# Performance work log

Measured on AMD Instinct MI355X. Metric: run time of the kernel, lower is better.

Reference implementation:

```python
import jax, jax.numpy as jnp
import numpy as np

B, IDF, CDF, IH, IW, SL = 32, 768, 768, 32, 32, 128

def setup_inputs() -> dict:
    key = jax.random.key(0)
    k1, k2, k3, k4 = jax.random.split(key, 4)
    inp = jax.random.normal(k1, (B, IDF, IH, IW), dtype=jnp.float32)
    ctx = jax.random.normal(k2, (B, CDF, SL), dtype=jnp.float32)
    mask = jax.random.randint(k3, (B, SL), 0, 2, dtype=jnp.int32)
    # 1x1 conv with no bias == matmul weight [idf, cdf]
    w_conv = jax.random.normal(k4, (IDF, CDF), dtype=jnp.float32) * 0.02
    return {"input": inp, "context": ctx, "mask": mask, "w_conv": w_conv}

def reference(input, context, mask, w_conv):
    b, idf, ih, iw = input.shape
    queryL = ih * iw
    sourceL = context.shape[2]
    # target: b x idf x queryL
    target = input.reshape(b, idf, queryL)
    # 1x1 conv projection of context: b x idf x sourceL
    sourceT = jnp.einsum('oc,bcs->bos', w_conv, context)
    # attention logits: b x queryL x sourceL (targetT @ sourceT)
    attn = jnp.einsum('biq,bis->bqs', target, sourceT)
    attn = attn + mask[:, None, :].astype(attn.dtype) * (-10000.0)
    attn = jax.nn.softmax(attn, axis=-1)  # softmax over sourceL
    # weighted context: sourceT @ attn^T -> b x idf x queryL
    weightedContext = jnp.einsum('bis,bqs->biq', sourceT, attn).reshape(b, idf, ih, iw)
    attn_out = jnp.transpose(attn, (0, 2, 1)).reshape(b, sourceL, ih, iw)
    return weightedContext, attn_out
```

## Files before the change

kernel.cpp:

```cpp
#include <hip/hip_runtime.h>

#define NB  32
#define IDF 768
#define SLN 128
#define QLN 1024
#define NT  24
#define NT2 12

typedef _Float16 v8hf __attribute__((ext_vector_type(8)));
typedef _Float16 v4hf __attribute__((ext_vector_type(4)));
typedef float    v4f  __attribute__((ext_vector_type(4)));

#define MFMAH __builtin_amdgcn_mfma_f32_16x16x32_f16

__device__ __forceinline__ void gload16(const void* g, void* l) {
  __builtin_amdgcn_global_load_lds(
      (const __attribute__((address_space(1))) void*)g,
      (__attribute__((address_space(3))) void*)l, 16, 0, 0);
}

__device__ __forceinline__ void lbar() {
  asm volatile("s_waitcnt lgkmcnt(0)" ::: "memory");
  __builtin_amdgcn_sched_barrier(0);
  __builtin_amdgcn_s_barrier();
  __builtin_amdgcn_sched_barrier(0);
}

__global__ __launch_bounds__(256) void prep_k(const float* __restrict__ W,
                                              const float* __restrict__ ctx,
                                              _Float16* __restrict__ Wf,
                                              _Float16* __restrict__ cTf) {
  const int bid = blockIdx.x, t = threadIdx.x;
  __shared__ float tl[64][133];
  if (bid < 576) {
    int idx = bid * 1024 + t * 4;
    float4 v = *(const float4*)(W + idx);
    v4hf h;
    h[0] = (_Float16)v.x;
    h[1] = (_Float16)v.y;
    h[2] = (_Float16)v.z;
    h[3] = (_Float16)v.w;
    *(v4hf*)(Wf + idx) = h;
    return;
  }
  const int cid = bid - 576;
  const int b = cid / 12, c0 = (cid % 12) * 64;
#pragma unroll
  for (int j = 0; j < 8; ++j) {
    int u = j * 256 + t;
    int c = u >> 5, s4 = (u & 31) * 4;
    *(float4*)&tl[c][s4] =
        *(const float4*)(ctx + ((size_t)b * IDF + c0 + c) * SLN + s4);
  }
  __syncthreads();
#pragma unroll
  for (int j = 0; j < 8; ++j) {
    int u = j * 256 + t;
    int s = u >> 4, c4 = (u & 15) * 4;
    v4hf h;
#pragma unroll
    for (int e = 0; e < 4; ++e) h[e] = (_Float16)tl[c4 + e][s];
    *(v4hf*)(cTf + ((size_t)b * SLN + s) * IDF + c0 + c4) = h;
  }
}

__global__ __launch_bounds__(256) void proj_k(const _Float16* __restrict__ cTf,
                                              const _Float16* __restrict__ Wf,
                                              _Float16* __restrict__ STf,
                                              _Float16* __restrict__ Shvf) {
  const int b = blockIdx.y, o0 = blockIdx.x * 32;
  const int t = threadIdx.x, w = t >> 6, lane = t & 63;
  const int lr = lane & 15, lg = lane >> 4;
  const int ws = w >> 1, wq = w & 1;
  __shared__ _Float16 AL[128][32];

  v4f acc[4];
#pragma unroll
  for (int fr = 0; fr < 4; ++fr) acc[fr] = (v4f){0.f, 0.f, 0.f, 0.f};

  const int ra = t >> 1, ca0 = (t & 1) * 2;
  const int swA = (ra >> 1) & 3;
  const int pa0 = (ca0 ^ swA) * 8, pa1 = ((ca0 + 1) ^ swA) * 8;
  const _Float16* pA = cTf + ((size_t)b * SLN + ra) * IDF + ca0 * 8;
  const size_t wOff = (size_t)(o0 + wq * 16 + lr) * IDF + lg * 8;

  uint4 aA0, aA1, bA0, bA1;
  v8hf bhc, bhn;
  aA0 = *(const uint4*)(pA);
  aA1 = *(const uint4*)(pA + 8);
  bA0 = *(const uint4*)(pA + 32);
  bA1 = *(const uint4*)(pA + 40);
  bhc = *(const v8hf*)(Wf + wOff);

#define PROJ_BODY(S0, S1, IT)                                                  \
  {                                                                            \
    lbar();                                                                    \
    *(uint4*)&AL[ra][pa0] = S0;                                                \
    *(uint4*)&AL[ra][pa1] = S1;                                                \
    if ((IT) + 2 < NT) {                                                       \
      S0 = *(const uint4*)(pA + ((IT) + 2) * 32);                              \
      S1 = *(const uint4*)(pA + ((IT) + 2) * 32 + 8);                          \
    }                                                                          \
    if ((IT) + 1 < NT) {                                                       \
      bhn = *(const v8hf*)(Wf + wOff + ((IT) + 1) * 32);                       \
    }                                                                          \
    lbar();                                                                    \
    _Pragma("unroll") for (int fr = 0; fr < 4; ++fr) {                         \
      const int r = ws * 64 + fr * 16 + lr;                                    \
      const int pp = (lg ^ ((r >> 1) & 3)) * 8;                                \
      v8hf ah = *(const v8hf*)&AL[r][pp];                                      \
      acc[fr] = MFMAH(ah, bhc, acc[fr], 0, 0, 0);                              \
    }                                                                          \
    bhc = bhn;                                                                 \
  }

  for (int it2 = 0; it2 < NT / 2; ++it2) {
    const int itE = it2 * 2;
    PROJ_BODY(aA0, aA1, itE);
    PROJ_BODY(bA0, bA1, itE + 1);
  }
#undef PROJ_BODY

  const int o = o0 + wq * 16 + lr;
#pragma unroll
  for (int fr = 0; fr < 4; ++fr) {
    v4hf hp;
#pragma unroll
    for (int r = 0; r < 4; ++r) {
      int s = ws * 64 + fr * 16 + lg * 4 + r;
      _Float16 h = (_Float16)acc[fr][r];
      STf[((size_t)b * SLN + s) * IDF + o] = h;
      hp[r] = h;
    }
    *(v4hf*)(Shvf + ((size_t)b * IDF + o) * SLN + ws * 64 + fr * 16 + lg * 4) =
        hp;
  }
}

__global__ __launch_bounds__(256, 4) void qkpv_k(const float* __restrict__ input,
                                                 const _Float16* __restrict__ STf,
                                                 const _Float16* __restrict__ Shvf,
                                                 const int* __restrict__ mask,
                                                 float* __restrict__ wc,
                                                 float* __restrict__ attn_out) {
  const int bid = blockIdx.x;
  const int nid = (bid & 7) * 64 + (bid >> 3);
  const int b = nid >> 4, q0 = (nid & 15) * 64;
  const int t = threadIdx.x, w = t >> 6, lane = t & 63;
  const int lr = lane & 15, lg = lane >> 4;
  const int wqp = w & 1, sh2 = w >> 1;

  __shared__ __align__(16) char lds[34304];
  float* const msk  = (float*)(lds + 32768);
  float* const redm = (float*)(lds + 33280);
  float* const reds = (float*)(lds + 33792);
  char* const PLb = lds;

  if (t < SLN) msk[t] = -10000.0f * (float)mask[b * SLN + t];

  v4f acc[4][2];
#pragma unroll
  for (int fr = 0; fr < 4; ++fr)
#pragma unroll
    for (int j = 0; j < 2; ++j) acc[fr][j] = (v4f){0.f, 0.f, 0.f, 0.f};

  const int rA = (lane >> 3);
  const int cpA = lane & 7;
  const _Float16* gA[4];
#pragma unroll
  for (int g = 0; g < 4; ++g) {
    const int row = w * 32 + g * 8 + rA;
    const int c = cpA ^ (row & 7);
    gA[g] = STf + ((size_t)b * SLN + row) * IDF + c * 8;
  }
  const int dA = w * 4096;

  const float* gB = input + (size_t)b * IDF * QLN + q0 + wqp * 32 + lr;

#pragma unroll
  for (int g = 0; g < 4; ++g) gload16(gA[g], lds + dA + g * 1024);
  v8hf aH[2][2], bH[2][2];
  float tmpB[2][2][8];
#pragma unroll
  for (int kk = 0; kk < 2; ++kk)
#pragma unroll
    for (int j = 0; j < 2; ++j)
#pragma unroll
      for (int e = 0; e < 8; ++e)
        tmpB[kk][j][e] = gB[(size_t)(kk * 32 + lg * 8 + e) * QLN + j * 16];
#pragma unroll
  for (int kk = 0; kk < 2; ++kk)
#pragma unroll
    for (int j = 0; j < 2; ++j)
#pragma unroll
      for (int e = 0; e < 8; ++e) aH[kk][j][e] = (_Float16)tmpB[kk][j][e];
#pragma unroll
  for (int g = 0; g < 4; ++g) gload16(gA[g] + 64, lds + 16384 + dA + g * 1024);

#define QK_WIN(CUROFF, BC, BN, IT, VMC)                                        \
  {                                                                            \
    asm volatile("s_waitcnt vmcnt(" #VMC ")" ::: "memory");                    \
    __builtin_amdgcn_sched_barrier(0);                                         \
    __builtin_amdgcn_s_barrier();                                              \
    __builtin_amdgcn_sched_barrier(0);                                         \
    if ((IT) + 1 < NT2) {                                                      \
      _Pragma("unroll") for (int kk = 0; kk < 2; ++kk)                         \
          _Pragma("unroll") for (int j = 0; j < 2; ++j)                        \
          _Pragma("unroll") for (int e = 0; e < 8; ++e)                        \
          tmpB[kk][j][e] =                                                     \
              gB[(size_t)(((IT) + 1) * 64 + kk * 32 + lg * 8 + e) * QLN +      \
                 j * 16];                                                      \
    }                                                                          \
    __builtin_amdgcn_sched_barrier(0);                                         \
    const char* Ab = lds + (CUROFF);                                           \
    __builtin_amdgcn_s_setprio(1);                                             \
    _Pragma("unroll") for (int fr = 0; fr < 4; ++fr) {                         \
      const int r = sh2 * 64 + fr * 16 + lr;                                   \
      _Pragma("unroll") for (int kk = 0; kk < 2; ++kk) {                       \
        const int cc = (kk * 4 + lg) ^ (r & 7);                                \
        v8hf ah = *(const v8hf*)(Ab + r * 128 + cc * 16);                      \
        _Pragma("unroll") for (int j = 0; j < 2; ++j) {                        \
          acc[fr][j] = MFMAH(ah, BC[kk][j], acc[fr][j], 0, 0, 0);              \
        }                                                                      \
      }                                                                        \
    }                                                                          \
    __builtin_amdgcn_s_setprio(0);                                             \
    __builtin_amdgcn_sched_barrier(0);                                         \
    if ((IT) + 1 < NT2) {                                                      \
      _Pragma("unroll") for (int kk = 0; kk < 2; ++kk)                         \
          _Pragma("unroll") for (int j = 0; j < 2; ++j)                        \
          _Pragma("unroll") for (int e = 0; e < 8; ++e)                        \
          BN[kk][j][e] = (_Float16)tmpB[kk][j][e];                             \
    }                                                                          \
    asm volatile("s_waitcnt lgkmcnt(0)" ::: "memory");                         \
    __builtin_amdgcn_s_barrier();                                              \
    if ((IT) + 2 < NT2) {                                                      \
      _Pragma("unroll") for (int g = 0; g < 4; ++g)                            \
          gload16(gA[g] + (size_t)((IT) + 2) * 64,                             \
                  lds + (CUROFF) + dA + g * 1024);                             \
    }                                                                          \
  }

  for (int it2 = 0; it2 < 5; ++it2) {
    const int itE = it2 * 2;
    QK_WIN(0, aH, bH, itE, 4);
    QK_WIN(16384, bH, aH, itE + 1, 4);
  }
  QK_WIN(0, aH, bH, 10, 4);
  QK_WIN(16384, bH, aH, 11, 0);
#undef QK_WIN

  float mx[2], sum[2];
#pragma unroll
  for (int j = 0; j < 2; ++j) {
    mx[j] = -3.0e38f;
#pragma unroll
    for (int fr = 0; fr < 4; ++fr)
#pragma unroll
      for (int r = 0; r < 4; ++r) {
        acc[fr][j][r] += msk[sh2 * 64 + fr * 16 + lg * 4 + r];
        mx[j] = fmaxf(mx[j], acc[fr][j][r]);
      }
    mx[j] = fmaxf(mx[j], __shfl_xor(mx[j], 16));
    mx[j] = fmaxf(mx[j], __shfl_xor(mx[j], 32));
    if (lg == 0) redm[sh2 * 64 + wqp * 32 + j * 16 + lr] = mx[j];
  }
  __syncthreads();
#pragma unroll
  for (int j = 0; j < 2; ++j) {
    const int qh = wqp * 32 + j * 16 + lr;
    mx[j] = fmaxf(redm[qh], redm[64 + qh]);
    sum[j] = 0.f;
#pragma unroll
    for (int fr = 0; fr < 4; ++fr)
#pragma unroll
      for (int r = 0; r < 4; ++r) {
        float e = __expf(acc[fr][j][r] - mx[j]);
        acc[fr][j][r] = e;
        sum[j] += e;
      }
    sum[j] += __shfl_xor(sum[j], 16);
    sum[j] += __shfl_xor(sum[j], 32);
    if (lg == 0) reds[sh2 * 64 + wqp * 32 + j * 16 + lr] = sum[j];
  }
  __syncthreads();
#pragma unroll
  for (int j = 0; j < 2; ++j) {
    const int qh = wqp * 32 + j * 16 + lr;
    const float inv = 1.0f / (reds[qh] + reds[64 + qh]);
    const int q = q0 + qh;
#pragma unroll
    for (int fr = 0; fr < 4; ++fr) {
      v4hf hp;
#pragma unroll
      for (int r = 0; r < 4; ++r) {
        float p = acc[fr][j][r] * inv;
        attn_out[((size_t)b * SLN + sh2 * 64 + fr * 16 + lg * 4 + r) * QLN + q] =
            p;
        hp[r] = (_Float16)p;
      }
      const int g = (sh2 * 8 + fr * 2 + (lg >> 1)) ^ lr;
      *(v4hf*)(PLb + qh * 256 + g * 16 + (lg & 1) * 8) = hp;
    }
  }
  __syncthreads();

  const int qfp = (w & 1) * 2;
  const int islab = (w >> 1) * 384;
  v8hf pa0v[4], pa1v[4];
#pragma unroll
  for (int kt = 0; kt < 4; ++kt) {
    const int g0 = (kt * 4 + lg) ^ lr;
    pa0v[kt] = *(const v8hf*)(PLb + (qfp * 16 + lr) * 256 + g0 * 16);
    pa1v[kt] = *(const v8hf*)(PLb + ((qfp + 1) * 16 + lr) * 256 + g0 * 16);
  }
  const _Float16* pShv = Shvf + ((size_t)b * IDF + islab + lr) * SLN + lg * 8;
  float* pWc = wc + ((size_t)b * IDF + islab + lr) * QLN + q0;
#pragma unroll 2
  for (int ifr = 0; ifr < 24; ++ifr) {
    v4f a0 = (v4f){0.f, 0.f, 0.f, 0.f};
    v4f a1 = (v4f){0.f, 0.f, 0.f, 0.f};
#pragma unroll
    for (int kt = 0; kt < 4; ++kt) {
      v8hf bb = *(const v8hf*)(pShv + (size_t)(ifr * 16) * SLN + kt * 32);
      a0 = MFMAH(pa0v[kt], bb, a0, 0, 0, 0);
      a1 = MFMAH(pa1v[kt], bb, a1, 0, 0, 0);
    }
    *(float4*)(pWc + (size_t)(ifr * 16) * QLN + qfp * 16 + lg * 4) =
        make_float4(a0[0], a0[1], a0[2], a0[3]);
    *(float4*)(pWc + (size_t)(ifr * 16) * QLN + (qfp + 1) * 16 + lg * 4) =
        make_float4(a1[0], a1[1], a1[2], a1[3]);
  }
}

extern "C" void kernel_launch(void* const* d_in, const int* in_sizes, int n_in,
                              void* d_out, int out_size, void* d_ws, size_t ws_size,
                              hipStream_t stream) {
  const float* input   = (const float*)d_in[0];
  const float* context = (const float*)d_in[1];
  const int*   mask    = (const int*)d_in[2];
  const float* w_conv  = (const float*)d_in[3];

  float* out      = (float*)d_out;
  float* wc       = out;
  float* attn_out = out + (size_t)NB * IDF * QLN;

  const size_t SE = (size_t)NB * SLN * IDF;
  _Float16* wsb = (_Float16*)d_ws;
  _Float16* STf  = wsb;
  _Float16* Shvf = STf + SE;
  _Float16* scr  = (_Float16*)wc;
  _Float16* cTf  = scr;
  _Float16* Wf   = cTf + SE;

  prep_k<<<960, 256, 0, stream>>>(w_conv, context, Wf, cTf);
  proj_k<<<dim3(24, NB), 256, 0, stream>>>(cTf, Wf, STf, Shvf);
  qkpv_k<<<512, 256, 0, stream>>>(input, STf, Shvf, mask, wc, attn_out);
}
```

Baseline: 81.16 us.

## Halve query tile per block to 32 and double grid to 1024 blocks

The fused QK-softmax-PV kernel now handles 32 query positions per block instead of 64, so the launch doubles to 1024 blocks and per-thread accumulators and B-fragment registers halve. This aims to raise occupancy and balance work across the many compute units. In exchange, each block reloads the full STf and Shvf slices for its batch, doubling their global/L2 traffic, and each block does fewer MFMAs per LDS/global load.

```diff
diff --git a/kernel.cpp b/kernel.cpp
--- a/kernel.cpp
+++ b/kernel.cpp
@@ -144,25 +144,23 @@
                                                  float* __restrict__ wc,
                                                  float* __restrict__ attn_out) {
   const int bid = blockIdx.x;
-  const int nid = (bid & 7) * 64 + (bid >> 3);
-  const int b = nid >> 4, q0 = (nid & 15) * 64;
+  const int nid = (bid & 7) * 128 + (bid >> 3);
+  const int b = nid >> 5, q0 = (nid & 31) * 32;
   const int t = threadIdx.x, w = t >> 6, lane = t & 63;
   const int lr = lane & 15, lg = lane >> 4;
-  const int wqp = w & 1, sh2 = w >> 1;
-
-  __shared__ __align__(16) char lds[34304];
+  const int wq = w & 1, sh2 = w >> 1;
+
+  __shared__ __align__(16) char lds[33792];
   float* const msk  = (float*)(lds + 32768);
   float* const redm = (float*)(lds + 33280);
-  float* const reds = (float*)(lds + 33792);
+  float* const reds = (float*)(lds + 33536);
   char* const PLb = lds;
 
   if (t < SLN) msk[t] = -10000.0f * (float)mask[b * SLN + t];
 
-  v4f acc[4][2];
-#pragma unroll
-  for (int fr = 0; fr < 4; ++fr)
-#pragma unroll
-    for (int j = 0; j < 2; ++j) acc[fr][j] = (v4f){0.f, 0.f, 0.f, 0.f};
+  v4f acc[4];
+#pragma unroll
+  for (int fr = 0; fr < 4; ++fr) acc[fr] = (v4f){0.f, 0.f, 0.f, 0.f};
 
   const int rA = (lane >> 3);
   const int cpA = lane & 7;
@@ -175,25 +173,21 @@
   }
   const int dA = w * 4096;
 
-  const float* gB = input + (size_t)b * IDF * QLN + q0 + wqp * 32 + lr;
+  const float* gB = input + (size_t)b * IDF * QLN + q0 + wq * 16 + lr;
 
 #pragma unroll
   for (int g = 0; g < 4; ++g) gload16(gA[g], lds + dA + g * 1024);
-  v8hf aH[2][2], bH[2][2];
-  float tmpB[2][2][8];
+  v8hf aH[2], bH[2];
+  float tmpB[2][8];
 #pragma unroll
   for (int kk = 0; kk < 2; ++kk)
 #pragma unroll
-    for (int j = 0; j < 2; ++j)
-#pragma unroll
-      for (int e = 0; e < 8; ++e)
-        tmpB[kk][j][e] = gB[(size_t)(kk * 32 + lg * 8 + e) * QLN + j * 16];
+    for (int e = 0; e < 8; ++e)
+      tmpB[kk][e] = gB[(size_t)(kk * 32 + lg * 8 + e) * QLN];
 #pragma unroll
   for (int kk = 0; kk < 2; ++kk)
 #pragma unroll
-    for (int j = 0; j < 2; ++j)
-#pragma unroll
-      for (int e = 0; e < 8; ++e) aH[kk][j][e] = (_Float16)tmpB[kk][j][e];
+    for (int e = 0; e < 8; ++e) aH[kk][e] = (_Float16)tmpB[kk][e];
 #pragma unroll
   for (int g = 0; g < 4; ++g) gload16(gA[g] + 64, lds + 16384 + dA + g * 1024);
 
@@ -205,11 +199,9 @@
     __builtin_amdgcn_sched_barrier(0);                                         \
     if ((IT) + 1 < NT2) {                                                      \
       _Pragma("unroll") for (int kk = 0; kk < 2; ++kk)                         \
-          _Pragma("unroll") for (int j = 0; j < 2; ++j)                        \
           _Pragma("unroll") for (int e = 0; e < 8; ++e)                        \
-          tmpB[kk][j][e] =                                                     \
-              gB[(size_t)(((IT) + 1) * 64 + kk * 32 + lg * 8 + e) * QLN +      \
-                 j * 16];                                                      \
+          tmpB[kk][e] =                                                        \
+              gB[(size_t)(((IT) + 1) * 64 + kk * 32 + lg * 8 + e) * QLN];      \
     }                                                                          \
     __builtin_amdgcn_sched_barrier(0);                                         \
     const char* Ab = lds + (CUROFF);                                           \
@@ -219,18 +211,15 @@
       _Pragma("unroll") for (int kk = 0; kk < 2; ++kk) {                       \
         const int cc = (kk * 4 + lg) ^ (r & 7);                                \
         v8hf ah = *(const v8hf*)(Ab + r * 128 + cc * 16);                      \
-        _Pragma("unroll") for (int j = 0; j < 2; ++j) {                        \
-          acc[fr][j] = MFMAH(ah, BC[kk][j], acc[fr][j], 0, 0, 0);              \
-        }                                                                      \
+        acc[fr] = MFMAH(ah, BC[kk], acc[fr], 0, 0, 0);                         \
       }                                                                        \
     }                                                                          \
     __builtin_amdgcn_s_setprio(0);                                             \
     __builtin_amdgcn_sched_barrier(0);                                         \
     if ((IT) + 1 < NT2) {                                                      \
       _Pragma("unroll") for (int kk = 0; kk < 2; ++kk)                         \
-          _Pragma("unroll") for (int j = 0; j < 2; ++j)                        \
           _Pragma("unroll") for (int e = 0; e < 8; ++e)                        \
-          BN[kk][j][e] = (_Float16)tmpB[kk][j][e];                             \
+          BN[kk][e] = (_Float16)tmpB[kk][e];                                   \
     }                                                                          \
     asm volatile("s_waitcnt lgkmcnt(0)" ::: "memory");                         \
     __builtin_amdgcn_s_barrier();                                              \
@@ -250,86 +239,69 @@
   QK_WIN(16384, bH, aH, 11, 0);
 #undef QK_WIN
 
-  float mx[2], sum[2];
-#pragma unroll
-  for (int j = 0; j < 2; ++j) {
-    mx[j] = -3.0e38f;
-#pragma unroll
-    for (int fr = 0; fr < 4; ++fr)
-#pragma unroll
-      for (int r = 0; r < 4; ++r) {
-        acc[fr][j][r] += msk[sh2 * 64 + fr * 16 + lg * 4 + r];
-        mx[j] = fmaxf(mx[j], acc[fr][j][r]);
-      }
-    mx[j] = fmaxf(mx[j], __shfl_xor(mx[j], 16));
-    mx[j] = fmaxf(mx[j], __shfl_xor(mx[j], 32));
-    if (lg == 0) redm[sh2 * 64 + wqp * 32 + j * 16 + lr] = mx[j];
-  }
+  const int qh = wq * 16 + lr;
+  float mx = -3.0e38f;
+#pragma unroll
+  for (int fr = 0; fr < 4; ++fr)
+#pragma unroll
+    for (int r = 0; r < 4; ++r) {
+      acc[fr][r] += msk[sh2 * 64 + fr * 16 + lg * 4 + r];
+      mx = fmaxf(mx, acc[fr][r]);
+    }
+  mx = fmaxf(mx, __shfl_xor(mx, 16));
+  mx = fmaxf(mx, __shfl_xor(mx, 32));
+  if (lg == 0) redm[sh2 * 32 + qh] = mx;
   __syncthreads();
-#pragma unroll
-  for (int j = 0; j < 2; ++j) {
-    const int qh = wqp * 32 + j * 16 + lr;
-    mx[j] = fmaxf(redm[qh], redm[64 + qh]);
-    sum[j] = 0.f;
-#pragma unroll
-    for (int fr = 0; fr < 4; ++fr)
-#pragma unroll
-      for (int r = 0; r < 4; ++r) {
-        float e = __expf(acc[fr][j][r] - mx[j]);
-        acc[fr][j][r] = e;
-        sum[j] += e;
-      }
-    sum[j] += __shfl_xor(sum[j], 16);
-    sum[j] += __shfl_xor(sum[j], 32);
-    if (lg == 0) reds[sh2 * 64 + wqp * 32 + j * 16 + lr] = sum[j];
-  }
+  mx = fmaxf(redm[qh], redm[32 + qh]);
+  float sum = 0.f;
+#pragma unroll
+  for (int fr = 0; fr < 4; ++fr)
+#pragma unroll
+    for (int r = 0; r < 4; ++r) {
+      float e = __expf(acc[fr][r] - mx);
+      acc[fr][r] = e;
+      sum += e;
+    }
+  sum += __shfl_xor(sum, 16);
+  sum += __shfl_xor(sum, 32);
+  if (lg == 0) reds[sh2 * 32 + qh] = sum;
   __syncthreads();
-#pragma unroll
-  for (int j = 0; j < 2; ++j) {
-    const int qh = wqp * 32 + j * 16 + lr;
-    const float inv = 1.0f / (reds[qh] + reds[64 + qh]);
-    const int q = q0 + qh;
-#pragma unroll
-    for (int fr = 0; fr < 4; ++fr) {
-      v4hf hp;
-#pragma unroll
-      for (int r = 0; r < 4; ++r) {
-        float p = acc[fr][j][r] * inv;
-        attn_out[((size_t)b * SLN + sh2 * 64 + fr * 16 + lg * 4 + r) * QLN + q] =
-            p;
-        hp[r] = (_Float16)p;
-      }
-      const int g = (sh2 * 8 + fr * 2 + (lg >> 1)) ^ lr;
-      *(v4hf*)(PLb + qh * 256 + g * 16 + (lg & 1) * 8) = hp;
-    }
+  const float inv = 1.0f / (reds[qh] + reds[32 + qh]);
+  const int q = q0 + qh;
+#pragma unroll
+  for (int fr = 0; fr < 4; ++fr) {
+    v4hf hp;
+#pragma unroll
+    for (int r = 0; r < 4; ++r) {
+      float p = acc[fr][r] * inv;
+      attn_out[((size_t)b * SLN + sh2 * 64 + fr * 16 + lg * 4 + r) * QLN + q] = p;
+      hp[r] = (_Float16)p;
+    }
+    const int g = (sh2 * 8 + fr * 2 + (lg >> 1)) ^ lr;
+    *(v4hf*)(PLb + qh * 256 + g * 16 + (lg & 1) * 8) = hp;
   }
   __syncthreads();
 
-  const int qfp = (w & 1) * 2;
+  const int qf = w & 1;
   const int islab = (w >> 1) * 384;
-  v8hf pa0v[4], pa1v[4];
+  v8hf pav[4];
 #pragma unroll
   for (int kt = 0; kt < 4; ++kt) {
     const int g0 = (kt * 4 + lg) ^ lr;
-    pa0v[kt] = *(const v8hf*)(PLb + (qfp * 16 + lr) * 256 + g0 * 16);
-    pa1v[kt] = *(const v8hf*)(PLb + ((qfp + 1) * 16 + lr) * 256 + g0 * 16);
+    pav[kt] = *(const v8hf*)(PLb + (qf * 16 + lr) * 256 + g0 * 16);
   }
   const _Float16* pShv = Shvf + ((size_t)b * IDF + islab + lr) * SLN + lg * 8;
-  float* pWc = wc + ((size_t)b * IDF + islab + lr) * QLN + q0;
-#pragma unroll 2
+  float* pWc = wc + ((size_t)b * IDF + islab + lr) * QLN + q0 + qf * 16 + lg * 4;
+#pragma unroll 4
   for (int ifr = 0; ifr < 24; ++ifr) {
     v4f a0 = (v4f){0.f, 0.f, 0.f, 0.f};
-    v4f a1 = (v4f){0.f, 0.f, 0.f, 0.f};
 #pragma unroll
     for (int kt = 0; kt < 4; ++kt) {
       v8hf bb = *(const v8hf*)(pShv + (size_t)(ifr * 16) * SLN + kt * 32);
-      a0 = MFMAH(pa0v[kt], bb, a0, 0, 0, 0);
-      a1 = MFMAH(pa1v[kt], bb, a1, 0, 0, 0);
-    }
-    *(float4*)(pWc + (size_t)(ifr * 16) * QLN + qfp * 16 + lg * 4) =
+      a0 = MFMAH(pav[kt], bb, a0, 0, 0, 0);
+    }
+    *(float4*)(pWc + (size_t)(ifr * 16) * QLN) =
         make_float4(a0[0], a0[1], a0[2], a0[3]);
-    *(float4*)(pWc + (size_t)(ifr * 16) * QLN + (qfp + 1) * 16 + lg * 4) =
-        make_float4(a1[0], a1[1], a1[2], a1[3]);
   }
 }
 
@@ -355,5 +327,5 @@
 
   prep_k<<<960, 256, 0, stream>>>(w_conv, context, Wf, cTf);
   proj_k<<<dim3(24, NB), 256, 0, stream>>>(cTf, Wf, STf, Shvf);
-  qkpv_k<<<512, 256, 0, stream>>>(input, STf, Shvf, mask, wc, attn_out);
-}
+  qkpv_k<<<1024, 256, 0, stream>>>(input, STf, Shvf, mask, wc, attn_out);
+}
```

Measured after the change: 101.9 us. 1.26x slower.
